# Optimization experiments

Hardware: AMD Instinct MI355X
Metric: run time of the kernel (lower is better)

## Reference

```python
import jax, jax.numpy as jnp
import numpy as np

EPS = 1e-7  # K.epsilon()
ROUTINGS = 3
NUM_CAPSULE = 8
FILTERS = 16


def squash(v, axis=-1):
    s2 = jnp.sum(jnp.square(v), axis=axis, keepdims=True)
    scale = s2 / (1.0 + s2) / jnp.sqrt(s2 + EPS)
    return scale * v


def _conv_per_caps(x, w):
    # x: [B,H,W,Cin], w: [k,k,Cin,Cout]
    return jax.lax.conv_general_dilated(
        x, w, window_strides=(1, 1), padding='SAME',
        dimension_numbers=('NHWC', 'HWIO', 'NHWC'))


def setup_inputs() -> dict:
    key = jax.random.key(0)
    k1, k2 = jax.random.split(key, 2)
    B, H, Wd, IN_CAPS, IN_F = 32, 32, 32, 8, 16
    input_tensor = jax.random.normal(k1, (B, H, Wd, IN_CAPS, IN_F), dtype=jnp.float32)
    # he_normal fan_in = k*k*Cin = 3*3*16 = 144
    W = jax.random.normal(k2, (IN_CAPS, 3, 3, IN_F, NUM_CAPSULE * FILTERS), dtype=jnp.float32) * np.sqrt(2.0 / 144.0)
    b = jnp.full((1, 1, NUM_CAPSULE, FILTERS), 0.1, dtype=jnp.float32)
    return {"input_tensor": input_tensor, "W": W, "b": b}


def reference(input_tensor, W, b):
    B, H, Wd, in_caps, in_f = input_tensor.shape
    # per-input-capsule conv: vmap over capsule axis of input and weight
    votes = jax.vmap(_conv_per_caps, in_axes=(3, 0), out_axes=1)(input_tensor, W)
    # [B, in_caps, H, W, num_cap*F] -> [B, in_caps, H, W, num_cap, F]
    votes = votes.reshape(B, in_caps, H, Wd, NUM_CAPSULE, FILTERS)

    # dynamic routing
    logits = jnp.zeros((B, in_caps, H, Wd, NUM_CAPSULE), dtype=votes.dtype)
    activation = None
    for i in range(ROUTINGS):
        route = jax.nn.softmax(logits, axis=-1)  # over output capsules
        # sum over input capsules of route-weighted votes, plus bias
        preactivate = jnp.einsum('bihwc,bihwcf->bhwcf', route, votes) + b
        activation = squash(preactivate, axis=-1)
        if i < ROUTINGS - 1:
            # scalar-product agreement
            logits = logits + jnp.einsum('bihwcf,bhwcf->bihwc', votes, activation)
    return activation.astype(jnp.float32)
```

## Files before the change

### kernel.cpp

```cpp
#include <hip/hip_runtime.h>
#include <math.h>


typedef _Float16 fp16x8 __attribute__((ext_vector_type(8)));
typedef float f32x4 __attribute__((ext_vector_type(4)));

#define EPS 1e-7f
constexpr int PSTRIDE = 136;
constexpr int LSTRIDE = 76;
constexpr int PXS     = 76;
constexpr int W_ELEMS = 40 * 8 * 64 * 8;

__device__ __forceinline__ float sumquad(float v) {
    v += __shfl_xor(v, 16);
    v += __shfl_xor(v, 32);
    return v;
}

__global__ __launch_bounds__(256)
void prep_weights(const float* __restrict__ wts,
                  _Float16* __restrict__ w16) {
    int n = blockIdx.x * 256 + threadIdx.x;
    if (n >= W_ELEMS) return;
    int j    = n & 7;
    int ln   = (n >> 3) & 63;
    int c0   = (n >> 9) & 7;
    int iq   = n >> 12;
    int i0   = iq / 5;
    int q0   = iq - i0 * 5;
    int k = q0 * 32 + (ln >> 4) * 8 + j;
    float w = 0.f;
    if (k < 144) w = wts[(i0 * 144 + k) * 128 + c0 * 16 + (ln & 15)];
    w16[n] = (_Float16)w;
}

__global__ __launch_bounds__(1024, 8)
void capsule_mfma_kernel(const float* __restrict__ x,
                         const _Float16* __restrict__ w16,
                         const float* __restrict__ bias,
                         float* __restrict__ out)
{
    __shared__ _Float16 patch[3 * 34 * PSTRIDE];
    __shared__ float lg_arr[32 * LSTRIDE];
    __shared__ float r_arr[32 * PXS];

    const int tid  = threadIdx.x;
    const int lane = tid & 63;
    const int wv   = tid >> 6;
    const int c    = wv & 7;
    const int Mt   = wv >> 3;
    const int l15  = lane & 15;
    const int quad = lane >> 4;
    const int lane8 = lane * 8;

    const int bid = blockIdx.x;
    const int h = bid & 31, b = bid >> 5;

    const float4* x4 = (const float4*)x;
    for (int idx = tid; idx < 102 * 32; idx += 1024) {
        int ch4  = idx & 31;
        int slot = idx >> 5;
        int row  = slot / 34;
        int colp = slot - row * 34;
        int gh = h - 1 + row;
        int gw = colp - 1;
        float4 v = {0.f, 0.f, 0.f, 0.f};
        if ((unsigned)gh < 32u && (unsigned)gw < 32u)
            v = x4[(((b * 32 + gh) * 32 + gw) << 5) + ch4];
        _Float16 ph[4];
        ph[0] = (_Float16)v.x; ph[1] = (_Float16)v.y;
        ph[2] = (_Float16)v.z; ph[3] = (_Float16)v.w;
        *(ushort4*)&patch[slot * PSTRIDE + ch4 * 4] = *(const ushort4*)ph;
    }
    __syncthreads();

    int a_off[5];
    #pragma unroll
    for (int q = 0; q < 5; ++q) {
        int tap = 2 * q + (quad >> 1);
        if (tap > 8) tap = 8;
        int dy = tap / 3, dx = tap - dy * 3;
        a_off[q] = (dy * 34 + (Mt * 16 + l15 + dx)) * PSTRIDE + (quad & 1) * 8;
    }

    f32x4 acc[8];
    #pragma unroll
    for (int i = 0; i < 8; ++i) acc[i] = (f32x4){0.f, 0.f, 0.f, 0.f};

    #pragma unroll
    for (int q = 0; q < 5; ++q) {
        #pragma unroll
        for (int i = 0; i < 8; ++i) {
            int woff = ((i * 5 + q) * 8 + c) * 512 + lane8;
            fp16x8 aw = *(const fp16x8*)(w16 + woff);
            fp16x8 bh = *(const fp16x8*)(patch + a_off[q] + i * 16);
            acc[i] = __builtin_amdgcn_mfma_f32_16x16x32_f16(aw, bh, acc[i], 0, 0, 0);
        }
    }

    const float4 bb4 = *(const float4*)(bias + c * 16 + quad * 4);
    const float barr[4] = {bb4.x, bb4.y, bb4.z, bb4.w};
    const int px = Mt * 16 + l15;

    float pre[4], actv[4];

    #pragma unroll
    for (int r = 0; r < 4; ++r) {
        float s = acc[0][r] + acc[1][r] + acc[2][r] + acc[3][r]
                + acc[4][r] + acc[5][r] + acc[6][r] + acc[7][r];
        pre[r] = s * 0.125f + barr[r];
    }
    {
        float s2 = sumquad(pre[0]*pre[0] + pre[1]*pre[1] + pre[2]*pre[2] + pre[3]*pre[3]);
        float scale = s2 * __builtin_amdgcn_rsqf(s2 + EPS) * __builtin_amdgcn_rcpf(1.f + s2);
        #pragma unroll
        for (int r = 0; r < 4; ++r) actv[r] = scale * pre[r];
    }
    #pragma unroll
    for (int i = 0; i < 8; ++i) {
        float t = acc[i][0]*actv[0] + acc[i][1]*actv[1]
                + acc[i][2]*actv[2] + acc[i][3]*actv[3];
        t = sumquad(t);
        if (quad == 0) lg_arr[px * LSTRIDE + i * 9 + c] = t;
    }
    __syncthreads();
    if (tid < 256) {
        int p = tid >> 3, ii = tid & 7;
        const float* lrow = &lg_arr[p * LSTRIDE + ii * 9];
        float m = lrow[0];
        #pragma unroll
        for (int cc = 1; cc < 8; ++cc) m = fmaxf(m, lrow[cc]);
        float e[8]; float den = 0.f;
        #pragma unroll
        for (int cc = 0; cc < 8; ++cc) { e[cc] = __expf(lrow[cc] - m); den += e[cc]; }
        float rd = __builtin_amdgcn_rcpf(den);
        #pragma unroll
        for (int cc = 0; cc < 8; ++cc) r_arr[p * PXS + cc * 8 + ii] = e[cc] * rd;
    }
    __syncthreads();

    {
        const float4* rp = (const float4*)&r_arr[px * PXS + c * 8];
        float4 r0 = rp[0], r1 = rp[1];
        #pragma unroll
        for (int r = 0; r < 4; ++r) {
            float s;
            s  = r0.x * acc[0][r]; s = fmaf(r0.y, acc[1][r], s);
            s  = fmaf(r0.z, acc[2][r], s); s = fmaf(r0.w, acc[3][r], s);
            s  = fmaf(r1.x, acc[4][r], s); s = fmaf(r1.y, acc[5][r], s);
            s  = fmaf(r1.z, acc[6][r], s); s = fmaf(r1.w, acc[7][r], s);
            pre[r] = s + barr[r];
        }
        float s2 = sumquad(pre[0]*pre[0] + pre[1]*pre[1] + pre[2]*pre[2] + pre[3]*pre[3]);
        float scale = s2 * __builtin_amdgcn_rsqf(s2 + EPS) * __builtin_amdgcn_rcpf(1.f + s2);
        #pragma unroll
        for (int r = 0; r < 4; ++r) actv[r] = scale * pre[r];
    }
    #pragma unroll
    for (int i = 0; i < 8; ++i) {
        float t = acc[i][0]*actv[0] + acc[i][1]*actv[1]
                + acc[i][2]*actv[2] + acc[i][3]*actv[3];
        t = sumquad(t);
        if (quad == 0) lg_arr[px * LSTRIDE + i * 9 + c] += t;
    }
    __syncthreads();
    if (tid < 256) {
        int p = tid >> 3, ii = tid & 7;
        const float* lrow = &lg_arr[p * LSTRIDE + ii * 9];
        float m = lrow[0];
        #pragma unroll
        for (int cc = 1; cc < 8; ++cc) m = fmaxf(m, lrow[cc]);
        float e[8]; float den = 0.f;
        #pragma unroll
        for (int cc = 0; cc < 8; ++cc) { e[cc] = __expf(lrow[cc] - m); den += e[cc]; }
        float rd = __builtin_amdgcn_rcpf(den);
        #pragma unroll
        for (int cc = 0; cc < 8; ++cc) r_arr[p * PXS + cc * 8 + ii] = e[cc] * rd;
    }
    __syncthreads();

    {
        const float4* rp = (const float4*)&r_arr[px * PXS + c * 8];
        float4 r0 = rp[0], r1 = rp[1];
        #pragma unroll
        for (int r = 0; r < 4; ++r) {
            float s;
            s  = r0.x * acc[0][r]; s = fmaf(r0.y, acc[1][r], s);
            s  = fmaf(r0.z, acc[2][r], s); s = fmaf(r0.w, acc[3][r], s);
            s  = fmaf(r1.x, acc[4][r], s); s = fmaf(r1.y, acc[5][r], s);
            s  = fmaf(r1.z, acc[6][r], s); s = fmaf(r1.w, acc[7][r], s);
            pre[r] = s + barr[r];
        }
        float s2 = sumquad(pre[0]*pre[0] + pre[1]*pre[1] + pre[2]*pre[2] + pre[3]*pre[3]);
        float scale = s2 * __builtin_amdgcn_rsqf(s2 + EPS) * __builtin_amdgcn_rcpf(1.f + s2);
        float4 o4 = { scale*pre[0], scale*pre[1], scale*pre[2], scale*pre[3] };
        *(float4*)(out + (((b * 32 + h) * 32 + px) << 7) + c * 16 + quad * 4) = o4;
    }
}

extern "C" void kernel_launch(void* const* d_in, const int* in_sizes, int n_in,
                              void* d_out, int out_size, void* d_ws, size_t ws_size,
                              hipStream_t stream) {
    const float* x    = (const float*)d_in[0];
    const float* wts  = (const float*)d_in[1];
    const float* bias = (const float*)d_in[2];
    float* out        = (float*)d_out;
    _Float16* w16     = (_Float16*)d_ws;

    prep_weights<<<dim3(640), dim3(256), 0, stream>>>(wts, w16);
    capsule_mfma_kernel<<<dim3(1024), dim3(1024), 0, stream>>>(x, w16, bias, out);
}
```

Measured before the change: 105.1 us.

## Halve block size and have each wave compute two M-tiles reusing weight fragments

Each block now uses 8 waves (512 threads) instead of 16. Each wave handles both 16-pixel halves of the row for its output capsule, so every weight fragment loaded from global memory feeds two MFMAs. This halves the redundant weight loads and the wave count per block. The cost is twice the accumulator registers per thread (64 floats), which may lower occupancy, and fewer waves are left to hide latency.

```diff
diff --git a/kernel.cpp b/kernel.cpp
--- a/kernel.cpp
+++ b/kernel.cpp
@@ -7,6 +7,7 @@
 
 #define EPS 1e-7f
 constexpr int PSTRIDE = 136;
+constexpr int PCOLS   = 34;
 constexpr int LSTRIDE = 76;
 constexpr int PXS     = 76;
 constexpr int W_ELEMS = 40 * 8 * 64 * 8;
@@ -34,21 +35,19 @@
     w16[n] = (_Float16)w;
 }
 
-__global__ __launch_bounds__(1024, 8)
+__global__ __launch_bounds__(512, 4)
 void capsule_mfma_kernel(const float* __restrict__ x,
                          const _Float16* __restrict__ w16,
                          const float* __restrict__ bias,
                          float* __restrict__ out)
 {
-    __shared__ _Float16 patch[3 * 34 * PSTRIDE];
+    __shared__ _Float16 patch[3 * PCOLS * PSTRIDE];
     __shared__ float lg_arr[32 * LSTRIDE];
     __shared__ float r_arr[32 * PXS];
 
     const int tid  = threadIdx.x;
     const int lane = tid & 63;
-    const int wv   = tid >> 6;
-    const int c    = wv & 7;
-    const int Mt   = wv >> 3;
+    const int c    = tid >> 6;
     const int l15  = lane & 15;
     const int quad = lane >> 4;
     const int lane8 = lane * 8;
@@ -57,11 +56,11 @@
     const int h = bid & 31, b = bid >> 5;
 
     const float4* x4 = (const float4*)x;
-    for (int idx = tid; idx < 102 * 32; idx += 1024) {
+    for (int idx = tid; idx < 3 * PCOLS * 32; idx += 512) {
         int ch4  = idx & 31;
         int slot = idx >> 5;
-        int row  = slot / 34;
-        int colp = slot - row * 34;
+        int row  = slot / PCOLS;
+        int colp = slot - row * PCOLS;
         int gh = h - 1 + row;
         int gw = colp - 1;
         float4 v = {0.f, 0.f, 0.f, 0.f};
@@ -80,12 +79,14 @@
         int tap = 2 * q + (quad >> 1);
         if (tap > 8) tap = 8;
         int dy = tap / 3, dx = tap - dy * 3;
-        a_off[q] = (dy * 34 + (Mt * 16 + l15 + dx)) * PSTRIDE + (quad & 1) * 8;
-    }
-
-    f32x4 acc[8];
-    #pragma unroll
-    for (int i = 0; i < 8; ++i) acc[i] = (f32x4){0.f, 0.f, 0.f, 0.f};
+        a_off[q] = (dy * PCOLS + l15 + dx) * PSTRIDE + (quad & 1) * 8;
+    }
+
+    f32x4 acc[2][8];
+    #pragma unroll
+    for (int mt = 0; mt < 2; ++mt)
+        #pragma unroll
+        for (int i = 0; i < 8; ++i) acc[mt][i] = (f32x4){0.f, 0.f, 0.f, 0.f};
 
     #pragma unroll
     for (int q = 0; q < 5; ++q) {
@@ -93,36 +94,41 @@
         for (int i = 0; i < 8; ++i) {
             int woff = ((i * 5 + q) * 8 + c) * 512 + lane8;
             fp16x8 aw = *(const fp16x8*)(w16 + woff);
-            fp16x8 bh = *(const fp16x8*)(patch + a_off[q] + i * 16);
-            acc[i] = __builtin_amdgcn_mfma_f32_16x16x32_f16(aw, bh, acc[i], 0, 0, 0);
+            fp16x8 b0 = *(const fp16x8*)(patch + a_off[q] + i * 16);
+            fp16x8 b1 = *(const fp16x8*)(patch + a_off[q] + 16 * PSTRIDE + i * 16);
+            acc[0][i] = __builtin_amdgcn_mfma_f32_16x16x32_f16(aw, b0, acc[0][i], 0, 0, 0);
+            acc[1][i] = __builtin_amdgcn_mfma_f32_16x16x32_f16(aw, b1, acc[1][i], 0, 0, 0);
         }
     }
 
     const float4 bb4 = *(const float4*)(bias + c * 16 + quad * 4);
     const float barr[4] = {bb4.x, bb4.y, bb4.z, bb4.w};
-    const int px = Mt * 16 + l15;
-
-    float pre[4], actv[4];
-
-    #pragma unroll
-    for (int r = 0; r < 4; ++r) {
-        float s = acc[0][r] + acc[1][r] + acc[2][r] + acc[3][r]
-                + acc[4][r] + acc[5][r] + acc[6][r] + acc[7][r];
-        pre[r] = s * 0.125f + barr[r];
-    }
-    {
+
+    float actv[2][4];
+
+    #pragma unroll
+    for (int mt = 0; mt < 2; ++mt) {
+        float pre[4];
+        #pragma unroll
+        for (int r = 0; r < 4; ++r) {
+            float s = acc[mt][0][r] + acc[mt][1][r] + acc[mt][2][r] + acc[mt][3][r]
+                    + acc[mt][4][r] + acc[mt][5][r] + acc[mt][6][r] + acc[mt][7][r];
+            pre[r] = s * 0.125f + barr[r];
+        }
         float s2 = sumquad(pre[0]*pre[0] + pre[1]*pre[1] + pre[2]*pre[2] + pre[3]*pre[3]);
         float scale = s2 * __builtin_amdgcn_rsqf(s2 + EPS) * __builtin_amdgcn_rcpf(1.f + s2);
         #pragma unroll
-        for (int r = 0; r < 4; ++r) actv[r] = scale * pre[r];
-    }
-    #pragma unroll
-    for (int i = 0; i < 8; ++i) {
-        float t = acc[i][0]*actv[0] + acc[i][1]*actv[1]
-                + acc[i][2]*actv[2] + acc[i][3]*actv[3];
-        t = sumquad(t);
-        if (quad == 0) lg_arr[px * LSTRIDE + i * 9 + c] = t;
-    }
+        for (int r = 0; r < 4; ++r) actv[mt][r] = scale * pre[r];
+    }
+    #pragma unroll
+    for (int mt = 0; mt < 2; ++mt)
+        #pragma unroll
+        for (int i = 0; i < 8; ++i) {
+            float t = acc[mt][i][0]*actv[mt][0] + acc[mt][i][1]*actv[mt][1]
+                    + acc[mt][i][2]*actv[mt][2] + acc[mt][i][3]*actv[mt][3];
+            t = sumquad(t);
+            if (quad == 0) lg_arr[(mt * 16 + l15) * LSTRIDE + i * 9 + c] = t;
+        }
     __syncthreads();
     if (tid < 256) {
         int p = tid >> 3, ii = tid & 7;
@@ -139,30 +145,34 @@
     }
     __syncthreads();
 
-    {
-        const float4* rp = (const float4*)&r_arr[px * PXS + c * 8];
+    #pragma unroll
+    for (int mt = 0; mt < 2; ++mt) {
+        const float4* rp = (const float4*)&r_arr[(mt * 16 + l15) * PXS + c * 8];
         float4 r0 = rp[0], r1 = rp[1];
+        float pre[4];
         #pragma unroll
         for (int r = 0; r < 4; ++r) {
             float s;
-            s  = r0.x * acc[0][r]; s = fmaf(r0.y, acc[1][r], s);
-            s  = fmaf(r0.z, acc[2][r], s); s = fmaf(r0.w, acc[3][r], s);
-            s  = fmaf(r1.x, acc[4][r], s); s = fmaf(r1.y, acc[5][r], s);
-            s  = fmaf(r1.z, acc[6][r], s); s = fmaf(r1.w, acc[7][r], s);
+            s  = r0.x * acc[mt][0][r]; s = fmaf(r0.y, acc[mt][1][r], s);
+            s  = fmaf(r0.z, acc[mt][2][r], s); s = fmaf(r0.w, acc[mt][3][r], s);
+            s  = fmaf(r1.x, acc[mt][4][r], s); s = fmaf(r1.y, acc[mt][5][r], s);
+            s  = fmaf(r1.z, acc[mt][6][r], s); s = fmaf(r1.w, acc[mt][7][r], s);
             pre[r] = s + barr[r];
         }
         float s2 = sumquad(pre[0]*pre[0] + pre[1]*pre[1] + pre[2]*pre[2] + pre[3]*pre[3]);
         float scale = s2 * __builtin_amdgcn_rsqf(s2 + EPS) * __builtin_amdgcn_rcpf(1.f + s2);
         #pragma unroll
-        for (int r = 0; r < 4; ++r) actv[r] = scale * pre[r];
-    }
-    #pragma unroll
-    for (int i = 0; i < 8; ++i) {
-        float t = acc[i][0]*actv[0] + acc[i][1]*actv[1]
-                + acc[i][2]*actv[2] + acc[i][3]*actv[3];
-        t = sumquad(t);
-        if (quad == 0) lg_arr[px * LSTRIDE + i * 9 + c] += t;
-    }
+        for (int r = 0; r < 4; ++r) actv[mt][r] = scale * pre[r];
+    }
+    #pragma unroll
+    for (int mt = 0; mt < 2; ++mt)
+        #pragma unroll
+        for (int i = 0; i < 8; ++i) {
+            float t = acc[mt][i][0]*actv[mt][0] + acc[mt][i][1]*actv[mt][1]
+                    + acc[mt][i][2]*actv[mt][2] + acc[mt][i][3]*actv[mt][3];
+            t = sumquad(t);
+            if (quad == 0) lg_arr[(mt * 16 + l15) * LSTRIDE + i * 9 + c] += t;
+        }
     __syncthreads();
     if (tid < 256) {
         int p = tid >> 3, ii = tid & 7;
@@ -179,21 +189,24 @@
     }
     __syncthreads();
 
-    {
-        const float4* rp = (const float4*)&r_arr[px * PXS + c * 8];
+    #pragma unroll
+    for (int mt = 0; mt < 2; ++mt) {
+        const float4* rp = (const float4*)&r_arr[(mt * 16 + l15) * PXS + c * 8];
         float4 r0 = rp[0], r1 = rp[1];
+        float pre[4];
         #pragma unroll
         for (int r = 0; r < 4; ++r) {
             float s;
-            s  = r0.x * acc[0][r]; s = fmaf(r0.y, acc[1][r], s);
-            s  = fmaf(r0.z, acc[2][r], s); s = fmaf(r0.w, acc[3][r], s);
-            s  = fmaf(r1.x, acc[4][r], s); s = fmaf(r1.y, acc[5][r], s);
-            s  = fmaf(r1.z, acc[6][r], s); s = fmaf(r1.w, acc[7][r], s);
+            s  = r0.x * acc[mt][0][r]; s = fmaf(r0.y, acc[mt][1][r], s);
+            s  = fmaf(r0.z, acc[mt][2][r], s); s = fmaf(r0.w, acc[mt][3][r], s);
+            s  = fmaf(r1.x, acc[mt][4][r], s); s = fmaf(r1.y, acc[mt][5][r], s);
+            s  = fmaf(r1.z, acc[mt][6][r], s); s = fmaf(r1.w, acc[mt][7][r], s);
             pre[r] = s + barr[r];
         }
         float s2 = sumquad(pre[0]*pre[0] + pre[1]*pre[1] + pre[2]*pre[2] + pre[3]*pre[3]);
         float scale = s2 * __builtin_amdgcn_rsqf(s2 + EPS) * __builtin_amdgcn_rcpf(1.f + s2);
         float4 o4 = { scale*pre[0], scale*pre[1], scale*pre[2], scale*pre[3] };
+        int px = mt * 16 + l15;
         *(float4*)(out + (((b * 32 + h) * 32 + px) << 7) + c * 16 + quad * 4) = o4;
     }
 }
@@ -208,5 +221,5 @@
     _Float16* w16     = (_Float16*)d_ws;
 
     prep_weights<<<dim3(640), dim3(256), 0, stream>>>(wts, w16);
-    capsule_mfma_kernel<<<dim3(1024), dim3(1024), 0, stream>>>(x, w16, bias, out);
-}
+    capsule_mfma_kernel<<<dim3(1024), dim3(512), 0, stream>>>(x, w16, bias, out);
+}
```

After: 102.8 us. -2.3%, faster.
